# Kernel optimization log

Hardware: AMD Instinct MI355X
Metric: run time of the kernel (lower is better)

The kernel has to match this reference:

```python
import jax, jax.numpy as jnp
import numpy as np

N_SRC = 50000
N_TGT = 50000
E = 1000000
D = 64                      # lifted_src = lifted_tgt = lifted_edge = global dim
MSG = 4 * D                 # message_dim = 256
LEAKY_SLOPE = 0.01


def setup_inputs() -> dict:
    key = jax.random.key(0)
    ks = jax.random.split(key, 10)
    x_s = jax.random.normal(ks[0], (N_SRC, D), dtype=jnp.float32)
    x_t = jax.random.normal(ks[1], (N_TGT, D), dtype=jnp.float32)
    edge_index = jax.random.randint(ks[2], (2, E), 0, N_SRC, dtype=jnp.int64)
    edge_attr = jax.random.normal(ks[3], (E, D), dtype=jnp.float32)
    x_u = jax.random.normal(ks[4], (D,), dtype=jnp.float32)
    # MLP params (torch Linear: y = x @ W.T + b; we store W as [in, out])
    s1 = 1.0 / np.sqrt(MSG)
    W1 = jax.random.uniform(ks[5], (MSG, MSG), jnp.float32, -s1, s1)
    b1 = jax.random.uniform(ks[6], (MSG,), jnp.float32, -s1, s1)
    W2 = jax.random.uniform(ks[7], (MSG, D), jnp.float32, -s1, s1)
    b2 = jax.random.uniform(ks[8], (D,), jnp.float32, -s1, s1)
    gamma = jnp.ones((D,), dtype=jnp.float32)  # RMSNorm weight
    return {"x_s": x_s, "x_t": x_t, "edge_index": edge_index,
            "edge_attr": edge_attr, "x_u": x_u,
            "W1": W1, "b1": b1, "W2": W2, "b2": b2, "gamma": gamma}


def reference(x_s, x_t, edge_index, edge_attr, x_u, W1, b1, W2, b2, gamma):
    src, tgt = edge_index[0], edge_index[1]
    e = edge_attr.shape[0]
    # gather + concat -> [E, MSG]
    h = jnp.concatenate(
        [x_s[src], x_t[tgt], edge_attr,
         jnp.broadcast_to(x_u, (e, x_u.shape[-1]))], axis=-1)
    # 2-layer MLP with LeakyReLU
    h = h @ W1 + b1
    h = jnp.where(h >= 0, h, LEAKY_SLOPE * h)
    h = h @ W2 + b2
    # RMSNorm (torch default eps = finfo(dtype).eps when eps=None)
    eps = jnp.finfo(h.dtype).eps
    rms = jax.lax.rsqrt(jnp.mean(h * h, axis=-1, keepdims=True) + eps)
    return h * rms * gamma
```

## Files before the change

kernel.cpp:

```cpp
#include <hip/hip_runtime.h>

typedef unsigned short ushort_t;
typedef unsigned int uint32;
typedef __bf16 bf16x8 __attribute__((ext_vector_type(8)));
typedef float floatx4 __attribute__((ext_vector_type(4)));

#define E_TOTAL 1000000
#define N_TILES 15625

__device__ __forceinline__ ushort_t f2bf(float f) {
  union { float f; uint32 i; } x; x.f = f;
  uint32 i = x.i;
  return (ushort_t)((i + 0x7fffu + ((i >> 16) & 1u)) >> 16);
}

__global__ void prep_kernel(const float* __restrict__ W1,
                            const float* __restrict__ W2,
                            const float* __restrict__ b1,
                            const float* __restrict__ xu,
                            ushort_t* __restrict__ W1p,
                            ushort_t* __restrict__ W2p,
                            float* __restrict__ bu1) {
  int bid = blockIdx.x;
  int tid = threadIdx.x;
  if (bid < 256) {
    int g = bid * 256 + tid;
    if (g < 49152) {
      int j = g & 7, l = (g >> 3) & 63, t = g >> 9;
      int kk = t >> 4, gnt = t & 15;
      int k = kk * 32 + ((l >> 4) * 8) + j;
      int n = gnt * 16 + (l & 15);
      W1p[g] = f2bf(W1[k * 256 + n]);
    } else {
      int g2 = g - 49152;
      int j = g2 & 7, l = (g2 >> 3) & 63, t = g2 >> 9;
      int kk = t >> 2, nt = t & 3;
      int k = kk * 32 + ((l >> 4) * 8) + j;
      int n = nt * 16 + (l & 15);
      W2p[g2] = f2bf(W2[k * 64 + n]);
    }
  } else {
    float s = b1[tid];
    for (int k = 0; k < 64; ++k)
      s += xu[k] * W1[(192 + k) * 256 + tid];
    bu1[tid] = s;
  }
}

__global__ __launch_bounds__(256, 2) void fused_kernel(
    const float* __restrict__ xs, const float* __restrict__ xt,
    const int* __restrict__ idx, const float* __restrict__ ea,
    const ushort_t* __restrict__ W1p, const ushort_t* __restrict__ W2p,
    const float* __restrict__ bu1, const float* __restrict__ b2,
    const float* __restrict__ gamma, float* __restrict__ out) {
  __shared__ uint4 lds_hp4[2048];
  __shared__ uint4 lds_w24[2048];
  char* lds_hp = (char*)lds_hp4;
  char* lds_w2 = (char*)lds_w24;

  const int tid  = threadIdx.x;
  const int wave = tid >> 6;
  const int lane = tid & 63;
  const int q    = lane >> 4;
  const int m16  = lane & 15;

  #pragma unroll
  for (int i = 0; i < 8; ++i)
    lds_w24[tid + i * 256] = ((const uint4*)W2p)[tid + i * 256];

  bf16x8 b1F[6][4];
  #pragma unroll
  for (int kk = 0; kk < 6; ++kk)
    #pragma unroll
    for (int n = 0; n < 4; ++n)
      b1F[kk][n] = ((const bf16x8*)W1p)[(kk * 16 + wave * 4 + n) * 64 + lane];

  float b1v[4], b2v[4], gv[4];
  #pragma unroll
  for (int n = 0; n < 4; ++n)
    b1v[n] = bu1[wave * 64 + n * 16 + m16];
  #pragma unroll
  for (int n = 0; n < 4; ++n) {
    b2v[n] = b2[n * 16 + m16];
    gv[n]  = gamma[n * 16 + m16];
  }

  const int r8  = tid >> 5;
  const int c   = tid & 31;
  const int seg = c >> 3;
  const int off = c & 7;

  for (int tile = blockIdx.x; tile < N_TILES; tile += gridDim.x) {
    const long e0 = (long)tile * 64;
    __syncthreads();

    if (c < 24) {
      #pragma unroll
      for (int p = 0; p < 8; ++p) {
        int r = p * 8 + r8;
        long e = e0 + r;
        const float4* sp;
        if (seg == 0)      sp = (const float4*)(xs + (size_t)idx[e] * 64);
        else if (seg == 1) sp = (const float4*)(xt + (size_t)idx[E_TOTAL + e] * 64);
        else               sp = (const float4*)(ea + (size_t)e * 64);
        float4 v0 = sp[off * 2];
        float4 v1 = sp[off * 2 + 1];
        uint4 o;
        o.x = (uint32)f2bf(v0.x) | ((uint32)f2bf(v0.y) << 16);
        o.y = (uint32)f2bf(v0.z) | ((uint32)f2bf(v0.w) << 16);
        o.z = (uint32)f2bf(v1.x) | ((uint32)f2bf(v1.y) << 16);
        o.w = (uint32)f2bf(v1.z) | ((uint32)f2bf(v1.w) << 16);
        int csw = c ^ (r & 7);
        *(uint4*)(lds_hp + r * 384 + csw * 16) = o;
      }
    }
    __syncthreads();

    floatx4 acc[4][4];
    #pragma unroll
    for (int mt = 0; mt < 4; ++mt)
      #pragma unroll
      for (int n = 0; n < 4; ++n)
        acc[mt][n] = (floatx4){0.f, 0.f, 0.f, 0.f};

    #pragma unroll
    for (int kk = 0; kk < 6; ++kk) {
      bf16x8 aF[4];
      #pragma unroll
      for (int mt = 0; mt < 4; ++mt) {
        int row = mt * 16 + m16;
        int ch  = (kk * 4 + q) ^ (row & 7);
        aF[mt] = *(const bf16x8*)(lds_hp + row * 384 + ch * 16);
      }
      #pragma unroll
      for (int mt = 0; mt < 4; ++mt)
        #pragma unroll
        for (int n = 0; n < 4; ++n)
          acc[mt][n] = __builtin_amdgcn_mfma_f32_16x16x32_bf16(
              aF[mt], b1F[kk][n], acc[mt][n], 0, 0, 0);
    }
    __syncthreads();

    #pragma unroll
    for (int mt = 0; mt < 4; ++mt)
      #pragma unroll
      for (int n = 0; n < 4; ++n)
        #pragma unroll
        for (int r = 0; r < 4; ++r) {
          float v = acc[mt][n][r] + b1v[n];
          v = (v >= 0.f) ? v : 0.01f * v;
          int row = mt * 16 + q * 4 + r;
          int col = (wave << 6) + n * 16 + m16;
          int ch  = (col >> 3) ^ (row & 7);
          *(ushort_t*)(lds_hp + row * 512 + ch * 16 + (col & 7) * 2) = f2bf(v);
        }
    __syncthreads();

    floatx4 acc2[4];
    #pragma unroll
    for (int n = 0; n < 4; ++n) acc2[n] = (floatx4){0.f, 0.f, 0.f, 0.f};

    #pragma unroll
    for (int kk = 0; kk < 8; ++kk) {
      int row = (wave << 4) + m16;
      int ch  = (kk * 4 + q) ^ (row & 7);
      bf16x8 a2 = *(const bf16x8*)(lds_hp + row * 512 + ch * 16);
      #pragma unroll
      for (int n = 0; n < 4; ++n) {
        bf16x8 bf = *(const bf16x8*)(lds_w2 + ((kk * 4 + n) * 64 + lane) * 16);
        acc2[n] = __builtin_amdgcn_mfma_f32_16x16x32_bf16(a2, bf, acc2[n], 0, 0, 0);
      }
    }

    float vals[4][4];
    #pragma unroll
    for (int n = 0; n < 4; ++n)
      #pragma unroll
      for (int r = 0; r < 4; ++r)
        vals[n][r] = acc2[n][r] + b2v[n];

    #pragma unroll
    for (int r = 0; r < 4; ++r) {
      float ss = 0.f;
      #pragma unroll
      for (int n = 0; n < 4; ++n) ss += vals[n][r] * vals[n][r];
      #pragma unroll
      for (int m = 1; m < 16; m <<= 1) ss += __shfl_xor(ss, m, 64);
      float rms = rsqrtf(ss * 0.015625f + 1.1920928955078125e-07f);
      long rowg = e0 + (wave << 4) + q * 4 + r;
      float* op = out + rowg * 64 + m16;
      #pragma unroll
      for (int n = 0; n < 4; ++n)
        op[n * 16] = vals[n][r] * rms * gv[n];
    }
  }
}

extern "C" void kernel_launch(void* const* d_in, const int* in_sizes, int n_in,
                              void* d_out, int out_size, void* d_ws, size_t ws_size,
                              hipStream_t stream) {
  const float* xs    = (const float*)d_in[0];
  const float* xt    = (const float*)d_in[1];
  const int*   idx   = (const int*)d_in[2];
  const float* ea    = (const float*)d_in[3];
  const float* xu    = (const float*)d_in[4];
  const float* W1    = (const float*)d_in[5];
  const float* b1    = (const float*)d_in[6];
  const float* W2    = (const float*)d_in[7];
  const float* b2    = (const float*)d_in[8];
  const float* gamma = (const float*)d_in[9];
  float* out = (float*)d_out;

  ushort_t* W1p = (ushort_t*)d_ws;
  ushort_t* W2p = W1p + 49152;
  float*    bu1 = (float*)((char*)d_ws + 131072);

  prep_kernel<<<257, 256, 0, stream>>>(W1, W2, b1, xu, W1p, W2p, bu1);
  fused_kernel<<<512, 256, 0, stream>>>(xs, xt, idx, ea, W1p, W2p, bu1, b2, gamma, out);
}
```

Measured before the change: 1.160 ms.

## Pre-convert node tables to bf16 and software-prefetch next tile's gathers

Adds a conversion pass that writes x_s and x_t as bf16 tables in workspace, halving the bytes fetched by the random node gathers. A new fused kernel prefetches the next tile's gathered rows and edge attributes into registers while the current tile runs its MLP, using explicit waitcnt and raw barriers to keep those loads in flight. It falls back to the old kernel when the workspace is too small. The cost is extra launches, a table conversion per call, and higher register pressure from the prefetch buffers.

Measured after the change: 1.021 ms. 1.14x faster.

```diff
diff --git a/kernel.cpp b/kernel.cpp
--- a/kernel.cpp
+++ b/kernel.cpp
@@ -7,6 +7,7 @@
 
 #define E_TOTAL 1000000
 #define N_TILES 15625
+#define N_NODES 50000
 
 __device__ __forceinline__ ushort_t f2bf(float f) {
   union { float f; uint32 i; } x; x.f = f;
@@ -47,6 +48,218 @@
   }
 }
 
+__global__ void conv_kernel(const float* __restrict__ src,
+                            ushort_t* __restrict__ dst, int n16) {
+  int i = blockIdx.x * 256 + threadIdx.x;
+  if (i >= n16) return;
+  const float4* s = (const float4*)src + (size_t)i * 2;
+  float4 a = s[0], b = s[1];
+  uint4 o;
+  o.x = (uint32)f2bf(a.x) | ((uint32)f2bf(a.y) << 16);
+  o.y = (uint32)f2bf(a.z) | ((uint32)f2bf(a.w) << 16);
+  o.z = (uint32)f2bf(b.x) | ((uint32)f2bf(b.y) << 16);
+  o.w = (uint32)f2bf(b.z) | ((uint32)f2bf(b.w) << 16);
+  ((uint4*)dst)[i] = o;
+}
+
+__device__ __forceinline__ void issue_pf(uint4 (&pf)[8], long e0n,
+    int c, int r8, int cj,
+    const ushort_t* __restrict__ xsb, const ushort_t* __restrict__ xtb,
+    const int* __restrict__ idx, const float* __restrict__ ea) {
+  if (c < 16) {
+    const ushort_t* tab = (c < 8) ? xsb : xtb;
+    const long base = (c < 8) ? 0 : (long)E_TOTAL;
+    int coff = c & 7;
+#pragma unroll
+    for (int p = 0; p < 8; ++p) {
+      int r = p * 8 + r8;
+      int id = idx[base + e0n + r];
+      pf[p] = *(const uint4*)(tab + (size_t)id * 64 + coff * 8);
+    }
+  } else {
+#pragma unroll
+    for (int p = 0; p < 8; ++p) {
+      int r = p * 8 + r8;
+      pf[p] = *(const uint4*)(ea + (size_t)(e0n + r) * 64 + (size_t)cj * 4);
+    }
+  }
+}
+
+#define WAIT_LGKM0() asm volatile("s_waitcnt lgkmcnt(0)" ::: "memory")
+#define RAW_BARRIER()                       \
+  do {                                      \
+    __builtin_amdgcn_sched_barrier(0);      \
+    __builtin_amdgcn_s_barrier();           \
+    __builtin_amdgcn_sched_barrier(0);      \
+  } while (0)
+
+__global__ __launch_bounds__(256, 2) void fused_pf_kernel(
+    const ushort_t* __restrict__ xsb, const ushort_t* __restrict__ xtb,
+    const int* __restrict__ idx, const float* __restrict__ ea,
+    const ushort_t* __restrict__ W1p, const ushort_t* __restrict__ W2p,
+    const float* __restrict__ bu1, const float* __restrict__ b2,
+    const float* __restrict__ gamma, float* __restrict__ out) {
+  __shared__ uint4 lds_hp4[2048];
+  __shared__ uint4 lds_w24[2048];
+  char* lds_hp = (char*)lds_hp4;
+  char* lds_w2 = (char*)lds_w24;
+
+  const int tid  = threadIdx.x;
+  const int wave = tid >> 6;
+  const int lane = tid & 63;
+  const int q    = lane >> 4;
+  const int m16  = lane & 15;
+
+#pragma unroll
+  for (int i = 0; i < 8; ++i)
+    lds_w24[tid + i * 256] = ((const uint4*)W2p)[tid + i * 256];
+
+  bf16x8 b1F[6][4];
+#pragma unroll
+  for (int kk = 0; kk < 6; ++kk)
+#pragma unroll
+    for (int n = 0; n < 4; ++n)
+      b1F[kk][n] = ((const bf16x8*)W1p)[(kk * 16 + wave * 4 + n) * 64 + lane];
+
+  float b1v[4], b2v[4], gv[4];
+#pragma unroll
+  for (int n = 0; n < 4; ++n)
+    b1v[n] = bu1[wave * 64 + n * 16 + m16];
+#pragma unroll
+  for (int n = 0; n < 4; ++n) {
+    b2v[n] = b2[n * 16 + m16];
+    gv[n]  = gamma[n * 16 + m16];
+  }
+
+  const int r8 = tid >> 5;
+  const int c  = tid & 31;
+  const int cj = c - 16;
+
+  uint4 pf[8];
+
+  __syncthreads();
+
+  issue_pf(pf, (long)blockIdx.x * 64, c, r8, cj, xsb, xtb, idx, ea);
+  asm volatile("s_waitcnt vmcnt(0)" ::: "memory");
+
+  for (int tile = blockIdx.x; tile < N_TILES; tile += gridDim.x) {
+    const long e0 = (long)tile * 64;
+
+    asm volatile("s_waitcnt vmcnt(16) lgkmcnt(0)" ::: "memory");
+    RAW_BARRIER();
+
+    if (c < 16) {
+#pragma unroll
+      for (int p = 0; p < 8; ++p) {
+        int r = p * 8 + r8;
+        int csw = c ^ (r & 7);
+        *(uint4*)(lds_hp + r * 384 + csw * 16) = pf[p];
+      }
+    } else {
+      int ch = 16 + (cj >> 1), ho = (cj & 1) * 8;
+#pragma unroll
+      for (int p = 0; p < 8; ++p) {
+        int r = p * 8 + r8;
+        float4 v = __builtin_bit_cast(float4, pf[p]);
+        uint2 o;
+        o.x = (uint32)f2bf(v.x) | ((uint32)f2bf(v.y) << 16);
+        o.y = (uint32)f2bf(v.z) | ((uint32)f2bf(v.w) << 16);
+        int csw = ch ^ (r & 7);
+        *(uint2*)(lds_hp + r * 384 + csw * 16 + ho) = o;
+      }
+    }
+
+    int tnext = tile + (int)gridDim.x;
+    if (tnext < N_TILES)
+      issue_pf(pf, (long)tnext * 64, c, r8, cj, xsb, xtb, idx, ea);
+
+    WAIT_LGKM0();
+    RAW_BARRIER();
+
+    floatx4 acc[4][4];
+#pragma unroll
+    for (int mt = 0; mt < 4; ++mt)
+#pragma unroll
+      for (int n = 0; n < 4; ++n)
+        acc[mt][n] = (floatx4){0.f, 0.f, 0.f, 0.f};
+
+#pragma unroll
+    for (int kk = 0; kk < 6; ++kk) {
+      bf16x8 aF[4];
+#pragma unroll
+      for (int mt = 0; mt < 4; ++mt) {
+        int row = mt * 16 + m16;
+        int ch  = (kk * 4 + q) ^ (row & 7);
+        aF[mt] = *(const bf16x8*)(lds_hp + row * 384 + ch * 16);
+      }
+#pragma unroll
+      for (int mt = 0; mt < 4; ++mt)
+#pragma unroll
+        for (int n = 0; n < 4; ++n)
+          acc[mt][n] = __builtin_amdgcn_mfma_f32_16x16x32_bf16(
+              aF[mt], b1F[kk][n], acc[mt][n], 0, 0, 0);
+    }
+
+    WAIT_LGKM0();
+    RAW_BARRIER();
+
+#pragma unroll
+    for (int mt = 0; mt < 4; ++mt)
+#pragma unroll
+      for (int n = 0; n < 4; ++n)
+#pragma unroll
+        for (int r = 0; r < 4; ++r) {
+          float v = acc[mt][n][r] + b1v[n];
+          v = (v >= 0.f) ? v : 0.01f * v;
+          int row = mt * 16 + q * 4 + r;
+          int col = (wave << 6) + n * 16 + m16;
+          int ch  = (col >> 3) ^ (row & 7);
+          *(ushort_t*)(lds_hp + row * 512 + ch * 16 + (col & 7) * 2) = f2bf(v);
+        }
+
+    WAIT_LGKM0();
+    RAW_BARRIER();
+
+    floatx4 acc2[4];
+#pragma unroll
+    for (int n = 0; n < 4; ++n) acc2[n] = (floatx4){0.f, 0.f, 0.f, 0.f};
+
+#pragma unroll
+    for (int kk = 0; kk < 8; ++kk) {
+      int row = (wave << 4) + m16;
+      int ch  = (kk * 4 + q) ^ (row & 7);
+      bf16x8 a2 = *(const bf16x8*)(lds_hp + row * 512 + ch * 16);
+#pragma unroll
+      for (int n = 0; n < 4; ++n) {
+        bf16x8 bf = *(const bf16x8*)(lds_w2 + ((kk * 4 + n) * 64 + lane) * 16);
+        acc2[n] = __builtin_amdgcn_mfma_f32_16x16x32_bf16(a2, bf, acc2[n], 0, 0, 0);
+      }
+    }
+
+    float vals[4][4];
+#pragma unroll
+    for (int n = 0; n < 4; ++n)
+#pragma unroll
+      for (int r = 0; r < 4; ++r)
+        vals[n][r] = acc2[n][r] + b2v[n];
+
+#pragma unroll
+    for (int r = 0; r < 4; ++r) {
+      float ss = 0.f;
+#pragma unroll
+      for (int n = 0; n < 4; ++n) ss += vals[n][r] * vals[n][r];
+#pragma unroll
+      for (int m = 1; m < 16; m <<= 1) ss += __shfl_xor(ss, m, 64);
+      float rms = rsqrtf(ss * 0.015625f + 1.1920928955078125e-07f);
+      long rowg = e0 + (wave << 4) + q * 4 + r;
+      float* op = out + rowg * 64 + m16;
+#pragma unroll
+      for (int n = 0; n < 4; ++n)
+        op[n * 16] = vals[n][r] * rms * gv[n];
+    }
+  }
+}
+
 __global__ __launch_bounds__(256, 2) void fused_kernel(
     const float* __restrict__ xs, const float* __restrict__ xt,
     const int* __restrict__ idx, const float* __restrict__ ea,
@@ -64,22 +277,22 @@
   const int q    = lane >> 4;
   const int m16  = lane & 15;
 
-  #pragma unroll
+#pragma unroll
   for (int i = 0; i < 8; ++i)
     lds_w24[tid + i * 256] = ((const uint4*)W2p)[tid + i * 256];
 
   bf16x8 b1F[6][4];
-  #pragma unroll
+#pragma unroll
   for (int kk = 0; kk < 6; ++kk)
-    #pragma unroll
+#pragma unroll
     for (int n = 0; n < 4; ++n)
       b1F[kk][n] = ((const bf16x8*)W1p)[(kk * 16 + wave * 4 + n) * 64 + lane];
 
   float b1v[4], b2v[4], gv[4];
-  #pragma unroll
+#pragma unroll
   for (int n = 0; n < 4; ++n)
     b1v[n] = bu1[wave * 64 + n * 16 + m16];
-  #pragma unroll
+#pragma unroll
   for (int n = 0; n < 4; ++n) {
     b2v[n] = b2[n * 16 + m16];
     gv[n]  = gamma[n * 16 + m16];
@@ -95,7 +308,7 @@
     __syncthreads();
 
     if (c < 24) {
-      #pragma unroll
+#pragma unroll
       for (int p = 0; p < 8; ++p) {
         int r = p * 8 + r8;
         long e = e0 + r;
@@ -117,35 +330,35 @@
     __syncthreads();
 
     floatx4 acc[4][4];
-    #pragma unroll
+#pragma unroll
     for (int mt = 0; mt < 4; ++mt)
-      #pragma unroll
+#pragma unroll
       for (int n = 0; n < 4; ++n)
         acc[mt][n] = (floatx4){0.f, 0.f, 0.f, 0.f};
 
-    #pragma unroll
+#pragma unroll
     for (int kk = 0; kk < 6; ++kk) {
       bf16x8 aF[4];
-      #pragma unroll
+#pragma unroll
       for (int mt = 0; mt < 4; ++mt) {
         int row = mt * 16 + m16;
         int ch  = (kk * 4 + q) ^ (row & 7);
         aF[mt] = *(const bf16x8*)(lds_hp + row * 384 + ch * 16);
       }
-      #pragma unroll
+#pragma unroll
       for (int mt = 0; mt < 4; ++mt)
-        #pragma unroll
+#pragma unroll
         for (int n = 0; n < 4; ++n)
           acc[mt][n] = __builtin_amdgcn_mfma_f32_16x16x32_bf16(
               aF[mt], b1F[kk][n], acc[mt][n], 0, 0, 0);
     }
     __syncthreads();
 
-    #pragma unroll
+#pragma unroll
     for (int mt = 0; mt < 4; ++mt)
-      #pragma unroll
-      for (int n = 0; n < 4; ++n)
-        #pragma unroll
+#pragma unroll
+      for (int n = 0; n < 4; ++n)
+#pragma unroll
         for (int r = 0; r < 4; ++r) {
           float v = acc[mt][n][r] + b1v[n];
           v = (v >= 0.f) ? v : 0.01f * v;
@@ -157,15 +370,15 @@
     __syncthreads();
 
     floatx4 acc2[4];
-    #pragma unroll
+#pragma unroll
     for (int n = 0; n < 4; ++n) acc2[n] = (floatx4){0.f, 0.f, 0.f, 0.f};
 
-    #pragma unroll
+#pragma unroll
     for (int kk = 0; kk < 8; ++kk) {
       int row = (wave << 4) + m16;
       int ch  = (kk * 4 + q) ^ (row & 7);
       bf16x8 a2 = *(const bf16x8*)(lds_hp + row * 512 + ch * 16);
-      #pragma unroll
+#pragma unroll
       for (int n = 0; n < 4; ++n) {
         bf16x8 bf = *(const bf16x8*)(lds_w2 + ((kk * 4 + n) * 64 + lane) * 16);
         acc2[n] = __builtin_amdgcn_mfma_f32_16x16x32_bf16(a2, bf, acc2[n], 0, 0, 0);
@@ -173,23 +386,23 @@
     }
 
     float vals[4][4];
-    #pragma unroll
+#pragma unroll
     for (int n = 0; n < 4; ++n)
-      #pragma unroll
+#pragma unroll
       for (int r = 0; r < 4; ++r)
         vals[n][r] = acc2[n][r] + b2v[n];
 
-    #pragma unroll
+#pragma unroll
     for (int r = 0; r < 4; ++r) {
       float ss = 0.f;
-      #pragma unroll
+#pragma unroll
       for (int n = 0; n < 4; ++n) ss += vals[n][r] * vals[n][r];
-      #pragma unroll
+#pragma unroll
       for (int m = 1; m < 16; m <<= 1) ss += __shfl_xor(ss, m, 64);
       float rms = rsqrtf(ss * 0.015625f + 1.1920928955078125e-07f);
       long rowg = e0 + (wave << 4) + q * 4 + r;
       float* op = out + rowg * 64 + m16;
-      #pragma unroll
+#pragma unroll
       for (int n = 0; n < 4; ++n)
         op[n * 16] = vals[n][r] * rms * gv[n];
     }
@@ -215,6 +428,23 @@
   ushort_t* W2p = W1p + 49152;
   float*    bu1 = (float*)((char*)d_ws + 131072);
 
+  const size_t TBL_OFF = 132096;
+  const size_t TBL_BYTES = (size_t)N_NODES * 64 * 2;
+  const size_t REQ = TBL_OFF + 2 * TBL_BYTES;
+
   prep_kernel<<<257, 256, 0, stream>>>(W1, W2, b1, xu, W1p, W2p, bu1);
-  fused_kernel<<<512, 256, 0, stream>>>(xs, xt, idx, ea, W1p, W2p, bu1, b2, gamma, out);
-}
+
+  if (ws_size >= REQ) {
+    ushort_t* xsb = (ushort_t*)((char*)d_ws + TBL_OFF);
+    ushort_t* xtb = xsb + (size_t)N_NODES * 64;
+    const int n16 = N_NODES * 64 / 8;
+    const int cgrid = (n16 + 255) / 256;
+    conv_kernel<<<cgrid, 256, 0, stream>>>(xs, xsb, n16);
+    conv_kernel<<<cgrid, 256, 0, stream>>>(xt, xtb, n16);
+    fused_pf_kernel<<<512, 256, 0, stream>>>(xsb, xtb, idx, ea, W1p, W2p,
+                                             bu1, b2, gamma, out);
+  } else {
+    fused_kernel<<<512, 256, 0, stream>>>(xs, xt, idx, ea, W1p, W2p,
+                                          bu1, b2, gamma, out);
+  }
+}
```
